# Kernel tuning notes

Measured on AMD Instinct MI355X. Metric: run time of the kernel, lower is better.

Reference implementation:

```python
import jax, jax.numpy as jnp
import numpy as np

B, L, D = 128, 512, 768   # batch, bert tokens, bert hidden
J = 32                    # clause boundaries -> S = J + 1 segments
S = J + 1
DM, DF = 200, 200         # transformer d_model / ffn dim
EPS = 1e-5


def _ln(x, g, b):
    m = x.mean(-1, keepdims=True)
    v = ((x - m) ** 2).mean(-1, keepdims=True)
    return (x - m) / jnp.sqrt(v + EPS) * g + b


def setup_inputs() -> dict:
    key = jax.random.key(0)
    ks = jax.random.split(key, 12)
    sc = 0.02
    hidden_state = jax.random.normal(ks[0], (B, L, D), jnp.float32)
    # strictly increasing, positive clause boundaries < L (non-empty segments)
    seg = L // S  # stride ~= 15 tokens per clause
    jitter = jax.random.randint(ks[1], (B, J), 0, seg).astype(jnp.int32)
    clause_idx = jnp.arange(1, J + 1, dtype=jnp.int32)[None, :] * seg + jitter
    p = lambda k, shp: sc * jax.random.normal(k, shp, jnp.float32)
    z = lambda n: jnp.zeros((n,), jnp.float32)
    return {
        'hidden_state': hidden_state,
        'clause_idx': clause_idx,
        'fc5_w': p(ks[2], (1, D)), 'fc5_b': z(1),
        'fc1_w': p(ks[3], (DM, D)), 'fc1_b': z(DM),
        'attn_in_w': p(ks[4], (3 * DM, DM)), 'attn_in_b': z(3 * DM),
        'attn_out_w': p(ks[5], (DM, DM)), 'attn_out_b': z(DM),
        'ln1_g': jnp.ones((DM,), jnp.float32), 'ln1_b': z(DM),
        'lin1_w': p(ks[6], (DF, DM)), 'lin1_b': z(DF),
        'lin2_w': p(ks[7], (DM, DF)), 'lin2_b': z(DM),
        'ln2_g': jnp.ones((DM,), jnp.float32), 'ln2_b': z(DM),
        'fc_w': p(ks[8], (2, 2 * DM)), 'fc_b': z(2),
    }


def reference(hidden_state, clause_idx, fc5_w, fc5_b, fc1_w, fc1_b,
              attn_in_w, attn_in_b, attn_out_w, attn_out_b,
              ln1_g, ln1_b, lin1_w, lin1_b, lin2_w, lin2_b,
              ln2_g, ln2_b, fc_w, fc_b):
    # ---- ragged per-segment attention pooling (batched_index_select) ----
    t = jnp.arange(L)
    # segment id of each token: number of boundaries <= t  -> [B, L] in [0, S)
    seg_id = jnp.sum(t[None, None, :] >= clause_idx[:, :, None], axis=1)
    scores = jnp.einsum('bld,d->bl', hidden_state, fc5_w[0]) + fc5_b[0]  # fc5
    mask = seg_id[:, None, :] == jnp.arange(S)[None, :, None]            # [B,S,L]
    logits = jnp.where(mask, scores[:, None, :], -jnp.inf)
    w = jax.nn.softmax(logits, axis=-1)        # per-segment softmax over tokens
    pooled = jnp.einsum('bsl,bld->bsd', w, hidden_state)                 # [B,S,D]

    # ---- fc1 + TransformerEncoderLayer (post-norm, 1 head, relu, no dropout)
    x = pooled @ fc1_w.T + fc1_b                                         # [B,S,DM]
    qkv = x @ attn_in_w.T + attn_in_b
    q, k, v = jnp.split(qkv, 3, axis=-1)
    a = jax.nn.softmax(jnp.einsum('bqd,bkd->bqk', q, k) * (1.0 / np.sqrt(DM).item()), axis=-1)
    att = jnp.einsum('bqk,bkd->bqd', a, v) @ attn_out_w.T + attn_out_b
    x = _ln(x + att, ln1_g, ln1_b)
    ff = jax.nn.relu(x @ lin1_w.T + lin1_b) @ lin2_w.T + lin2_b
    x = _ln(x + ff, ln2_g, ln2_b)

    # ---- cat(first-token broadcast, rest) then classifier fc ----
    h = jnp.concatenate([jnp.broadcast_to(x[:, :1, :], (B, S - 1, DM)), x[:, 1:, :]], axis=-1)
    return h @ fc_w.T + fc_b                                             # [B, S-1, 2]
```

## Files before the change

kernel.cpp:

```cpp
#include <hip/hip_runtime.h>

#define NB 128
#define LL 512
#define DD 768
#define JJ 32
#define SS 33
#define DM 200

typedef __attribute__((ext_vector_type(8))) short bf8_t;
typedef __attribute__((ext_vector_type(4))) float f4_t;

#define SB_XF   0
#define SB_QB   61440
#define SB_KB   82944
#define SB_VT   104448
#define SB_Y2   235520
#define SB_BLK  275456

static __device__ __forceinline__ unsigned short f2bf(float f) {
  unsigned u = __float_as_uint(f);
  return (unsigned short)((u + 0x7FFFu + ((u >> 16) & 1u)) >> 16);
}

template<int KS>
static __device__ __forceinline__ f4_t mfma_tile(
    const unsigned short* pa, const unsigned short* pw)
{
  f4_t acc = {0.f, 0.f, 0.f, 0.f};
  bf8_t a = *(const bf8_t*)pa;
  bf8_t w = *(const bf8_t*)pw;
#pragma unroll
  for (int s = 1; s < KS; ++s) {
    bf8_t a2 = *(const bf8_t*)(pa + 32 * s);
    bf8_t w2 = *(const bf8_t*)(pw + 32 * s);
    acc = __builtin_amdgcn_mfma_f32_16x16x32_bf16(a, w, acc, 0, 0, 0);
    a = a2; w = w2;
  }
  acc = __builtin_amdgcn_mfma_f32_16x16x32_bf16(a, w, acc, 0, 0, 0);
  return acc;
}

template<int KS>
static __device__ __forceinline__ f4_t mfma_tile_lds(
    const unsigned short* pa, const unsigned short* pw)
{
  f4_t acc = {0.f, 0.f, 0.f, 0.f};
#pragma unroll
  for (int s = 0; s < KS; ++s) {
    bf8_t a = *(const bf8_t*)(pa + 32 * s);
    bf8_t w = *(const bf8_t*)(pw + 32 * s);
    acc = __builtin_amdgcn_mfma_f32_16x16x32_bf16(a, w, acc, 0, 0, 0);
  }
  return acc;
}

__global__ __launch_bounds__(512) void pc_kernel(
    const float* __restrict__ hidden, const int* __restrict__ clause,
    const float* __restrict__ fc5w, unsigned short* __restrict__ pooled_bf,
    const float* __restrict__ fc1_w, const float* __restrict__ ain_w,
    const float* __restrict__ aout_w, const float* __restrict__ lin1_w,
    const float* __restrict__ lin2_w,
    unsigned short* __restrict__ fc1_wb, unsigned short* __restrict__ ain_wb,
    unsigned short* __restrict__ aout_wb, unsigned short* __restrict__ lin1_wb,
    unsigned short* __restrict__ lin2_wb, char* __restrict__ scratch)
{
  const int tid = threadIdx.x;
  if (blockIdx.x >= NB * SS) {
    int t = (blockIdx.x - NB * SS) * 512 + tid;
    if (t < 208 * 768) {
      int n = t / 768, k = t - n * 768;
      fc1_wb[t] = f2bf((n < 200) ? fc1_w[n * 768 + k] : 0.f);
      return;
    }
    t -= 208 * 768;
    if (t < 608 * 224) {
      int n = t / 224, k = t - n * 224;
      ain_wb[t] = f2bf((n < 600 && k < 200) ? ain_w[n * 200 + k] : 0.f);
      return;
    }
    t -= 608 * 224;
    if (t < 208 * 224) {
      int n = t / 224, k = t - n * 224;
      aout_wb[t] = f2bf((n < 200 && k < 200) ? aout_w[n * 200 + k] : 0.f);
      return;
    }
    t -= 208 * 224;
    if (t < 208 * 224) {
      int n = t / 224, k = t - n * 224;
      lin1_wb[t] = f2bf((n < 200 && k < 200) ? lin1_w[n * 200 + k] : 0.f);
      return;
    }
    t -= 208 * 224;
    if (t < 208 * 224) {
      int n = t / 224, k = t - n * 224;
      lin2_wb[t] = f2bf((n < 200 && k < 200) ? lin2_w[n * 200 + k] : 0.f);
      return;
    }
    t -= 208 * 224;
    if (t < NB * 1344) {
      int b = t / 1344, r = t - b * 1344;
      char* sb = scratch + (size_t)b * SB_BLK;
      const uint4 z = make_uint4(0, 0, 0, 0);
      if (r < 384) {
        int bi = r / 192, rr = r - bi * 192;
        int row = rr >> 2, c = rr & 3;
        int off = (bi == 0) ? SB_QB : SB_KB;
        *(uint4*)((unsigned short*)(sb + off) + row * 224 + 192 + c * 8) = z;
      } else {
        int rr = r - 384;
        int row = rr >> 2, c = rr & 3;
        *(uint4*)((unsigned short*)(sb + SB_VT) + row * 64 + 32 + c * 8) = z;
      }
    }
    return;
  }

  int blk = blockIdx.x;
  int b = blk / SS;
  int s = blk - b * SS;
  int t0 = (s == 0) ? 0 : clause[b * JJ + s - 1];
  int t1 = (s == JJ) ? LL : clause[b * JJ + s];
  int nt = t1 - t0;
  if (nt > 64) nt = 64;
  if (nt < 1) nt = 1;

  __shared__ float wsm[64];
  int wave = tid >> 6, lane = tid & 63;

  const float4* w4 = (const float4*)fc5w;
  float4 wa = w4[lane], wwb = w4[lane + 64], wc = w4[lane + 128];
  for (int t = t0 + wave; t < t0 + nt; t += 8) {
    const float4* hp = (const float4*)(hidden + ((long long)b * LL + t) * DD);
    float4 h0 = hp[lane], h1 = hp[lane + 64], h2 = hp[lane + 128];
    float acc = h0.x*wa.x + h0.y*wa.y + h0.z*wa.z + h0.w*wa.w
              + h1.x*wwb.x + h1.y*wwb.y + h1.z*wwb.z + h1.w*wwb.w
              + h2.x*wc.x + h2.y*wc.y + h2.z*wc.z + h2.w*wc.w;
#pragma unroll
    for (int off = 32; off; off >>= 1) acc += __shfl_xor(acc, off);
    if (lane == 0) wsm[t - t0] = acc;
  }
  __syncthreads();

  if (wave == 0) {
    float v = (lane < nt) ? wsm[lane] : -__builtin_inff();
    float mx = v;
#pragma unroll
    for (int off = 32; off; off >>= 1) mx = fmaxf(mx, __shfl_xor(mx, off));
    float e = (lane < nt) ? __expf(v - mx) : 0.f;
    float sm = e;
#pragma unroll
    for (int off = 32; off; off >>= 1) sm += __shfl_xor(sm, off);
    if (lane < nt) wsm[lane] = e / sm;
  }
  __syncthreads();

  if (tid < 384) {
    const float2* base = (const float2*)(hidden + ((long long)b * LL + t0) * DD);
    float2 acc = make_float2(0.f, 0.f);
#pragma unroll 4
    for (int t = 0; t < nt; ++t) {
      float w = wsm[t];
      float2 h = base[t * 384 + tid];
      acc.x = fmaf(w, h.x, acc.x);
      acc.y = fmaf(w, h.y, acc.y);
    }
    ushort2 o;
    o.x = f2bf(acc.x); o.y = f2bf(acc.y);
    *(ushort2*)(pooled_bf + (long long)blk * DD + tid * 2) = o;
  }
}

__global__ __launch_bounds__(512, 4) void k_fc1qkv(
    const unsigned short* __restrict__ pooled,
    const unsigned short* __restrict__ fc1_wb, const float* __restrict__ fc1_b,
    const unsigned short* __restrict__ ain_wb, const float* __restrict__ ain_b,
    char* __restrict__ scratch)
{
  const int b = blockIdx.x / 3, mt = blockIdx.x % 3, m0 = mt * 16;
  const int tid = threadIdx.x, wv = tid >> 6, lane = tid & 63;
  const int col = lane & 15, quad = lane >> 4, koff = quad * 8;

  char* sb = scratch + (size_t)b * SB_BLK;
  float* x_f32 = (float*)(sb + SB_XF);
  unsigned short* q_bf  = (unsigned short*)(sb + SB_QB);
  unsigned short* k_bf  = (unsigned short*)(sb + SB_KB);
  unsigned short* vt_bf = (unsigned short*)(sb + SB_VT);

  __shared__ __align__(16) unsigned short sA[16][776];
  __shared__ __align__(16) unsigned short xb[16][232];

  {
    int r = tid >> 5, c = tid & 31;
    int src = m0 + r; if (src > 32) src = 32;
    const unsigned* gp = (const unsigned*)(pooled + (size_t)(b * SS + src) * DD);
    unsigned* lp = (unsigned*)&sA[r][0];
#pragma unroll
    for (int i = 0; i < 12; ++i) lp[c + 32 * i] = gp[c + 32 * i];
  }
  for (int u = tid; u < 16 * 16; u += 512) {
    int row = u >> 4, c = u & 15;
    ((unsigned*)&xb[row][200])[c] = 0u;
  }
  __syncthreads();

  for (int t = wv; t < 13; t += 8) {
    int n0 = t * 16;
    f4_t acc = mfma_tile_lds<24>(&sA[0][0] + col * 776 + koff,
                                 fc1_wb + (size_t)(n0 + col) * DD + koff);
    int gn = n0 + col;
    if (gn < DM) {
      float bv = fc1_b[gn];
#pragma unroll
      for (int r = 0; r < 4; ++r) {
        int row = quad * 4 + r;
        float v = acc[r] + bv;
        x_f32[(m0 + row) * 208 + gn] = v;
        xb[row][gn] = f2bf(v);
      }
    }
  }
  __syncthreads();

  for (int t = wv; t < 38; t += 8) {
    int n0 = t * 16;
    f4_t acc = mfma_tile_lds<7>(&xb[0][0] + col * 232 + koff,
                                ain_wb + (size_t)(n0 + col) * 224 + koff);
    int gn = n0 + col;
    if (gn < 600) {
      float bv = ain_b[gn];
#pragma unroll
      for (int r = 0; r < 4; ++r) {
        int gm = m0 + quad * 4 + r;
        unsigned short bfv = f2bf(acc[r] + bv);
        if (gn < 200)      q_bf[gm * 224 + gn] = bfv;
        else if (gn < 400) k_bf[gm * 224 + (gn - 200)] = bfv;
        else if (gm < SS)  vt_bf[(gn - 400) * 64 + gm] = bfv;
      }
    }
  }
}

__global__ __launch_bounds__(512, 4) void k_postattn(
    const unsigned short* __restrict__ aout_wb, const float* __restrict__ aout_b,
    const float* __restrict__ ln1_g, const float* __restrict__ ln1_b,
    const unsigned short* __restrict__ lin1_wb, const float* __restrict__ lin1_b,
    const unsigned short* __restrict__ lin2_wb, const float* __restrict__ lin2_b,
    const float* __restrict__ ln2_g, const float* __restrict__ ln2_b,
    char* __restrict__ scratch)
{
  const int b = blockIdx.x / 3, mt = blockIdx.x % 3, m0 = mt * 16;
  const int tid = threadIdx.x, wv = tid >> 6, lane = tid & 63;
  const int col = lane & 15, quad = lane >> 4, koff = quad * 8;

  char* sb = scratch + (size_t)b * SB_BLK;
  const unsigned short* q_bf  = (const unsigned short*)(sb + SB_QB);
  const unsigned short* k_bf  = (const unsigned short*)(sb + SB_KB);
  const unsigned short* vt_bf = (const unsigned short*)(sb + SB_VT);
  const float* x_f32 = (const float*)(sb + SB_XF);
  float* y2g = (float*)(sb + SB_Y2);

  __shared__ float tc[16][211];
  __shared__ __align__(16) unsigned short Pb[16][72];
  __shared__ __align__(16) unsigned short yb[16][232];
  __shared__ __align__(16) unsigned short fb[16][232];
  for (int u = tid; u < 16 * 16; u += 512) {
    int row = u >> 4, c = u & 15;
    ((unsigned*)&yb[row][200])[c] = 0u;
    ((unsigned*)&fb[row][200])[c] = 0u;
  }

  for (int t = wv; t < 3; t += 8) {
    int n0 = t * 16;
    f4_t acc = mfma_tile<7>(q_bf + (m0 + col) * 224 + koff,
                            k_bf + (n0 + col) * 224 + koff);
    int gn = n0 + col;
#pragma unroll
    for (int r = 0; r < 4; ++r)
      tc[quad * 4 + r][gn] = acc[r] * 0.07071067811865475f;
  }
  __syncthreads();

  for (int r = wv; r < 16; r += 8) {
    bool live = (m0 + r) < SS;
    float v = (lane < SS && live) ? tc[r][lane] : -__builtin_inff();
    float mx = v;
#pragma unroll
    for (int off = 32; off; off >>= 1) mx = fmaxf(mx, __shfl_xor(mx, off));
    float e = (lane < SS && live) ? __expf(v - mx) : 0.f;
    float sm = e;
#pragma unroll
    for (int off = 32; off; off >>= 1) sm += __shfl_xor(sm, off);
    Pb[r][lane] = (lane < SS && live) ? f2bf(e / sm) : (unsigned short)0;
  }
  __syncthreads();

  for (int t = wv; t < 13; t += 8) {
    int n0 = t * 16;
    f4_t acc = mfma_tile_lds<2>(&Pb[0][0] + col * 72 + koff,
                                vt_bf + (n0 + col) * 64 + koff);
    int gn = n0 + col;
    if (gn < DM) {
#pragma unroll
      for (int r = 0; r < 4; ++r)
        fb[quad * 4 + r][gn] = f2bf(acc[r]);
    }
  }
  __syncthreads();

  for (int t = wv; t < 13; t += 8) {
    int n0 = t * 16;
    f4_t acc = mfma_tile_lds<7>(&fb[0][0] + col * 232 + koff,
                                aout_wb + (size_t)(n0 + col) * 224 + koff);
    int gn = n0 + col;
    float bv = (gn < DM) ? aout_b[gn] : 0.f;
#pragma unroll
    for (int r = 0; r < 4; ++r) {
      int row = quad * 4 + r;
      float v = acc[r] + bv;
      if (gn < DM) v += x_f32[(m0 + row) * 208 + gn];
      tc[row][gn] = v;
    }
  }
  __syncthreads();

  for (int r = wv; r < 16; r += 8) {
    float* p = &tc[r][0];
    float vals[4]; float s = 0.f;
#pragma unroll
    for (int i = 0; i < 4; ++i) { int k = lane + 64 * i; vals[i] = (k < DM) ? p[k] : 0.f; s += vals[i]; }
#pragma unroll
    for (int off = 32; off; off >>= 1) s += __shfl_xor(s, off);
    float mean = s * (1.f / DM);
    float vs = 0.f;
#pragma unroll
    for (int i = 0; i < 4; ++i) { int k = lane + 64 * i; if (k < DM) { float d = vals[i] - mean; vs += d * d; } }
#pragma unroll
    for (int off = 32; off; off >>= 1) vs += __shfl_xor(vs, off);
    float rstd = rsqrtf(vs * (1.f / DM) + 1e-5f);
#pragma unroll
    for (int i = 0; i < 4; ++i) {
      int k = lane + 64 * i;
      if (k < DM) {
        float o = (vals[i] - mean) * rstd * ln1_g[k] + ln1_b[k];
        p[k] = o;
        yb[r][k] = f2bf(o);
      }
    }
  }
  __syncthreads();

  for (int t = wv; t < 13; t += 8) {
    int n0 = t * 16;
    f4_t acc = mfma_tile_lds<7>(&yb[0][0] + col * 232 + koff,
                                lin1_wb + (size_t)(n0 + col) * 224 + koff);
    int gn = n0 + col;
    if (gn < DM) {
      float bv = lin1_b[gn];
#pragma unroll
      for (int r = 0; r < 4; ++r)
        fb[quad * 4 + r][gn] = f2bf(fmaxf(acc[r] + bv, 0.f));
    }
  }
  __syncthreads();

  for (int t = wv; t < 13; t += 8) {
    int n0 = t * 16;
    f4_t acc = mfma_tile_lds<7>(&fb[0][0] + col * 232 + koff,
                                lin2_wb + (size_t)(n0 + col) * 224 + koff);
    int gn = n0 + col;
    if (gn < DM) {
      float bv = lin2_b[gn];
#pragma unroll
      for (int r = 0; r < 4; ++r) {
        int row = quad * 4 + r;
        tc[row][gn] = acc[r] + bv + tc[row][gn];
      }
    }
  }
  __syncthreads();

  for (int r = wv; r < 16; r += 8) {
    float* p = &tc[r][0];
    float vals[4]; float s = 0.f;
#pragma unroll
    for (int i = 0; i < 4; ++i) { int k = lane + 64 * i; vals[i] = (k < DM) ? p[k] : 0.f; s += vals[i]; }
#pragma unroll
    for (int off = 32; off; off >>= 1) s += __shfl_xor(s, off);
    float mean = s * (1.f / DM);
    float vs = 0.f;
#pragma unroll
    for (int i = 0; i < 4; ++i) { int k = lane + 64 * i; if (k < DM) { float d = vals[i] - mean; vs += d * d; } }
#pragma unroll
    for (int off = 32; off; off >>= 1) vs += __shfl_xor(vs, off);
    float rstd = rsqrtf(vs * (1.f / DM) + 1e-5f);
    int grow = m0 + r;
#pragma unroll
    for (int i = 0; i < 4; ++i) {
      int k = lane + 64 * i;
      if (k < DM) y2g[grow * 208 + k] = (vals[i] - mean) * rstd * ln2_g[k] + ln2_b[k];
    }
  }
}

__global__ __launch_bounds__(256) void k_cls(
    const char* __restrict__ scratch, const float* __restrict__ fcw,
    const float* __restrict__ fcb, float* __restrict__ out)
{
  int gw = blockIdx.x * 4 + (threadIdx.x >> 6);
  int lane = threadIdx.x & 63;
  int b = gw >> 5, j = gw & 31;
  const float* y2 = (const float*)(scratch + (size_t)b * SB_BLK + SB_Y2);
  const float* r0 = y2;
  const float* rj = y2 + (1 + j) * 208;
  float a0 = 0.f, a1 = 0.f;
  for (int k = lane; k < DM; k += 64) {
    float u = r0[k], w = rj[k];
    a0 += u * fcw[k]       + w * fcw[200 + k];
    a1 += u * fcw[400 + k] + w * fcw[600 + k];
  }
#pragma unroll
  for (int off = 32; off; off >>= 1) {
    a0 += __shfl_xor(a0, off);
    a1 += __shfl_xor(a1, off);
  }
  if (lane == 0) {
    out[gw * 2 + 0] = a0 + fcb[0];
    out[gw * 2 + 1] = a1 + fcb[1];
  }
}

extern "C" void kernel_launch(void* const* d_in, const int* in_sizes, int n_in,
                              void* d_out, int out_size, void* d_ws, size_t ws_size,
                              hipStream_t stream)
{
  (void)in_sizes; (void)n_in; (void)out_size; (void)ws_size;
  const float* hidden = (const float*)d_in[0];
  const int*   clause = (const int*)d_in[1];
  const float* fc5_w  = (const float*)d_in[2];
  const float* fc1_w  = (const float*)d_in[4];
  const float* fc1_b  = (const float*)d_in[5];
  const float* ain_w  = (const float*)d_in[6];
  const float* ain_b  = (const float*)d_in[7];
  const float* aout_w = (const float*)d_in[8];
  const float* aout_b = (const float*)d_in[9];
  const float* ln1_g  = (const float*)d_in[10];
  const float* ln1_b  = (const float*)d_in[11];
  const float* lin1_w = (const float*)d_in[12];
  const float* lin1_b = (const float*)d_in[13];
  const float* lin2_w = (const float*)d_in[14];
  const float* lin2_b = (const float*)d_in[15];
  const float* ln2_g  = (const float*)d_in[16];
  const float* ln2_b  = (const float*)d_in[17];
  const float* fc_w   = (const float*)d_in[18];
  const float* fc_b   = (const float*)d_in[19];
  float* out = (float*)d_out;

  char* w8 = (char*)d_ws;
  unsigned short* pooled_bf = (unsigned short*)(w8 + 0);
  char* scratch = w8 + 6520832;
  size_t wbase = 6520832 + (size_t)NB * SB_BLK;
  unsigned short* fc1_wb  = (unsigned short*)(w8 + wbase);
  unsigned short* ain_wb  = (unsigned short*)(w8 + wbase + 319488);
  unsigned short* aout_wb = (unsigned short*)(w8 + wbase + 591872);
  unsigned short* lin1_wb = (unsigned short*)(w8 + wbase + 685056);
  unsigned short* lin2_wb = (unsigned short*)(w8 + wbase + 778240);

  pc_kernel<<<dim3(NB * SS + 1187), 512, 0, stream>>>(
      hidden, clause, fc5_w, pooled_bf,
      fc1_w, ain_w, aout_w, lin1_w, lin2_w,
      fc1_wb, ain_wb, aout_wb, lin1_wb, lin2_wb, scratch);
  k_fc1qkv<<<dim3(NB * 3), 512, 0, stream>>>(pooled_bf, fc1_wb, fc1_b,
      ain_wb, ain_b, scratch);
  k_postattn<<<dim3(NB * 3), 512, 0, stream>>>(aout_wb, aout_b, ln1_g, ln1_b,
      lin1_wb, lin1_b, lin2_wb, lin2_b, ln2_g, ln2_b, scratch);
  k_cls<<<dim3(1024), 256, 0, stream>>>(scratch, fc_w, fc_b, out);
}
```

Before: 374.7 us.

## Keep segment hidden rows in registers for pooling instead of re-reading global memory

The pooling kernel used to read each segment's hidden rows twice: once for the fc5 scores and again for the weighted sum. The rows for the first 32 tokens per segment now stay in registers, so each wave computes its own partial weighted sum, and the partials are reduced across waves through a new LDS buffer. This roughly halves global traffic on the dominant hidden-state read. The cost is much higher register use per thread, an extra LDS buffer of about 25 KB, and one more barrier. The launch bounds also add a minimum of 4 blocks per SM, which may cause spilling.

```diff
diff --git a/kernel.cpp b/kernel.cpp
--- a/kernel.cpp
+++ b/kernel.cpp
@@ -54,7 +54,7 @@
   return acc;
 }
 
-__global__ __launch_bounds__(512) void pc_kernel(
+__global__ __launch_bounds__(512, 4) void pc_kernel(
     const float* __restrict__ hidden, const int* __restrict__ clause,
     const float* __restrict__ fc5w, unsigned short* __restrict__ pooled_bf,
     const float* __restrict__ fc1_w, const float* __restrict__ ain_w,
@@ -125,19 +125,37 @@
   if (nt < 1) nt = 1;
 
   __shared__ float wsm[64];
+  __shared__ __align__(16) float pw[8][772];
   int wave = tid >> 6, lane = tid & 63;
 
   const float4* w4 = (const float4*)fc5w;
   float4 wa = w4[lane], wwb = w4[lane + 64], wc = w4[lane + 128];
-  for (int t = t0 + wave; t < t0 + nt; t += 8) {
-    const float4* hp = (const float4*)(hidden + ((long long)b * LL + t) * DD);
+
+  float4 hv[4][3];
+#pragma unroll
+  for (int i = 0; i < 4; ++i) {
+    int r = wave + 8 * i;
+    if (r < nt) {
+      const float4* hp = (const float4*)(hidden + ((long long)b * LL + t0 + r) * DD);
+      float4 h0 = hp[lane], h1 = hp[lane + 64], h2 = hp[lane + 128];
+      hv[i][0] = h0; hv[i][1] = h1; hv[i][2] = h2;
+      float acc = h0.x*wa.x + h0.y*wa.y + h0.z*wa.z + h0.w*wa.w
+                + h1.x*wwb.x + h1.y*wwb.y + h1.z*wwb.z + h1.w*wwb.w
+                + h2.x*wc.x + h2.y*wc.y + h2.z*wc.z + h2.w*wc.w;
+#pragma unroll
+      for (int off = 32; off; off >>= 1) acc += __shfl_xor(acc, off);
+      if (lane == 0) wsm[r] = acc;
+    }
+  }
+  for (int r = wave + 32; r < nt; r += 8) {
+    const float4* hp = (const float4*)(hidden + ((long long)b * LL + t0 + r) * DD);
     float4 h0 = hp[lane], h1 = hp[lane + 64], h2 = hp[lane + 128];
     float acc = h0.x*wa.x + h0.y*wa.y + h0.z*wa.z + h0.w*wa.w
               + h1.x*wwb.x + h1.y*wwb.y + h1.z*wwb.z + h1.w*wwb.w
               + h2.x*wc.x + h2.y*wc.y + h2.z*wc.z + h2.w*wc.w;
 #pragma unroll
     for (int off = 32; off; off >>= 1) acc += __shfl_xor(acc, off);
-    if (lane == 0) wsm[t - t0] = acc;
+    if (lane == 0) wsm[r] = acc;
   }
   __syncthreads();
 
@@ -154,15 +172,43 @@
   }
   __syncthreads();
 
+  float4 p0 = {0,0,0,0}, p1 = {0,0,0,0}, p2 = {0,0,0,0};
+#pragma unroll
+  for (int i = 0; i < 4; ++i) {
+    int r = wave + 8 * i;
+    if (r < nt) {
+      float w = wsm[r];
+      p0.x = fmaf(w, hv[i][0].x, p0.x); p0.y = fmaf(w, hv[i][0].y, p0.y);
+      p0.z = fmaf(w, hv[i][0].z, p0.z); p0.w = fmaf(w, hv[i][0].w, p0.w);
+      p1.x = fmaf(w, hv[i][1].x, p1.x); p1.y = fmaf(w, hv[i][1].y, p1.y);
+      p1.z = fmaf(w, hv[i][1].z, p1.z); p1.w = fmaf(w, hv[i][1].w, p1.w);
+      p2.x = fmaf(w, hv[i][2].x, p2.x); p2.y = fmaf(w, hv[i][2].y, p2.y);
+      p2.z = fmaf(w, hv[i][2].z, p2.z); p2.w = fmaf(w, hv[i][2].w, p2.w);
+    }
+  }
+  for (int r = wave + 32; r < nt; r += 8) {
+    const float4* hp = (const float4*)(hidden + ((long long)b * LL + t0 + r) * DD);
+    float w = wsm[r];
+    float4 h0 = hp[lane], h1 = hp[lane + 64], h2 = hp[lane + 128];
+    p0.x = fmaf(w, h0.x, p0.x); p0.y = fmaf(w, h0.y, p0.y);
+    p0.z = fmaf(w, h0.z, p0.z); p0.w = fmaf(w, h0.w, p0.w);
+    p1.x = fmaf(w, h1.x, p1.x); p1.y = fmaf(w, h1.y, p1.y);
+    p1.z = fmaf(w, h1.z, p1.z); p1.w = fmaf(w, h1.w, p1.w);
+    p2.x = fmaf(w, h2.x, p2.x); p2.y = fmaf(w, h2.y, p2.y);
+    p2.z = fmaf(w, h2.z, p2.z); p2.w = fmaf(w, h2.w, p2.w);
+  }
+  {
+    float4* pp = (float4*)&pw[wave][0];
+    pp[lane] = p0; pp[lane + 64] = p1; pp[lane + 128] = p2;
+  }
+  __syncthreads();
+
   if (tid < 384) {
-    const float2* base = (const float2*)(hidden + ((long long)b * LL + t0) * DD);
     float2 acc = make_float2(0.f, 0.f);
-#pragma unroll 4
-    for (int t = 0; t < nt; ++t) {
-      float w = wsm[t];
-      float2 h = base[t * 384 + tid];
-      acc.x = fmaf(w, h.x, acc.x);
-      acc.y = fmaf(w, h.y, acc.y);
+#pragma unroll
+    for (int w = 0; w < 8; ++w) {
+      float2 v = *(const float2*)&pw[w][tid * 2];
+      acc.x += v.x; acc.y += v.y;
     }
     ushort2 o;
     o.x = f2bf(acc.x); o.y = f2bf(acc.y);
```

New measurement: 367.6 us. No clear change (-1.9%).
